# Kernel optimization log

Hardware: AMD Instinct MI355X
Metric: run time of the kernel (lower is better)

The kernel has to match this reference:

```python
import jax, jax.numpy as jnp
import numpy as np

EPS = 1e-9
LDIM = 4  # dim_g + dim_t + dim_b + dim_w


def _mvn_logpdf(v, F):
    # batched zero-mean multivariate normal log-density, v: (N,O), F: (N,O,O)
    chol = jnp.linalg.cholesky(F)
    z = jax.scipy.linalg.solve_triangular(chol, v[..., None], lower=True)[..., 0]
    quad = jnp.sum(z * z, axis=-1)
    logdet = 2.0 * jnp.sum(jnp.log(jnp.diagonal(chol, axis1=-2, axis2=-1)), axis=-1)
    k = v.shape[-1]
    return -0.5 * (quad + logdet + k * jnp.log(2.0 * jnp.pi))


def _forward(y, B_G, B_T, B_B, B_W, lambda_r1_free, lambda_r2_free,
             q_diag, r_diag, gamma1, gamma2_learnable):
    N, Nt, O = y.shape
    L = LDIM
    # ----- _build_matrices -----
    B11 = jnp.zeros((L, L)).at[0, 0].set(B_G[0, 0]).at[1, 1].set(B_T[0, 0]).at[2, 2].set(B_B[0, 0])
    B22 = jnp.zeros((L, L)).at[3, 3].set(B_W[0, 0])
    B12 = jnp.zeros((L, L)).at[3, :3].set(1.0 / 3.0)  # regime1 factors feed shared factor
    B21 = jnp.zeros((L, L))
    L1 = jnp.zeros((O, L))
    L1 = L1.at[0, 0].set(1.0).at[1, 0].set(lambda_r1_free[0]).at[2, 0].set(lambda_r1_free[1])
    L1 = L1.at[3, 1].set(1.0).at[4, 1].set(lambda_r1_free[2]).at[5, 1].set(lambda_r1_free[3])
    L1 = L1.at[6, 2].set(1.0).at[7, 2].set(lambda_r1_free[4]).at[8, 2].set(lambda_r1_free[5])
    L2 = jnp.zeros((O, L)).at[0, 3].set(1.0).at[1:, 3].set(lambda_r2_free)
    Q = jnp.diag(jnp.abs(q_diag) + 1e-4)
    R = jnp.diag(jnp.abs(r_diag) + 1e-4)
    F_JIT = 1e-5 * jnp.eye(O)
    I_L = jnp.eye(L)
    P22_CONST = 0.9999

    # ----- initial beliefs ('informative') -----
    prob0 = jnp.tile(jnp.array([0.99, 0.01], jnp.float32), (N, 1))
    eta0 = jnp.zeros((N, L), y.dtype)
    P0 = jnp.tile(jnp.diag(jnp.array([1000.0, 1000.0, 1000.0, 1e-9], y.dtype))[None], (N, 1, 1))

    def predict(B, eta, P):
        # eta: (N,L), P: (N,L,L)
        return eta @ B.T, jnp.einsum('ij,njk,lk->nil', B, P, B) + Q

    def innov(Lm, e, Pp, y_t):
        v = y_t - e @ Lm.T
        F = jnp.einsum('oi,nij,pj->nop', Lm, Pp, Lm) + R + F_JIT
        return v, F

    def kupdate(e, Pp, Lm, v, F):
        LP = jnp.einsum('oi,nij->noj', Lm, Pp)          # (N,O,L)
        K = jnp.swapaxes(jnp.linalg.solve(F, LP), -1, -2)  # P Lm^T F^{-1}, (N,L,O)
        e_u = e + jnp.einsum('nlo,no->nl', K, v)
        IKL = I_L - K @ Lm                                # (N,L,L)
        P_u = IKL @ Pp @ jnp.swapaxes(IKL, -1, -2) + jnp.einsum('nlo,op,nmp->nlm', K, R, K)
        return e_u, P_u

    def collapse(w_a, w_b, e_a, e_b, P_a, P_b):
        e = w_a[:, None] * e_a + w_b[:, None] * e_b
        da, db = e_a - e, e_b - e
        P = (w_a[:, None, None] * (P_a + da[:, :, None] * da[:, None, :])
             + w_b[:, None, None] * (P_b + db[:, :, None] * db[:, None, :]))
        return e, P

    def step(carry, y_t):
        prob, eta1, eta2, P1, P2, ll = carry
        # HMM transition: p11 depends on regime-1 state (first L-1 components)
        logit_p11 = gamma1 + eta1[:, :3] @ gamma2_learnable
        p11 = jax.nn.sigmoid(logit_p11)
        # predictions for the 4 regime transitions (origin -> destination)
        e11, Pp11 = predict(B11, eta1, P1)
        e12, Pp12 = predict(B21, eta2, P2)
        e21, Pp21 = predict(B12, eta1, P1)
        e22, Pp22 = predict(B22, eta2, P2)
        v11, F11 = innov(L1, e11, Pp11, y_t)
        v12, F12 = innov(L1, e12, Pp12, y_t)
        v21, F21 = innov(L2, e21, Pp21, y_t)
        v22, F22 = innov(L2, e22, Pp22, y_t)
        ll11 = _mvn_logpdf(v11, F11)
        ll12 = _mvn_logpdf(v12, F12)
        ll21 = _mvn_logpdf(v21, F21)
        ll22 = _mvn_logpdf(v22, F22)
        lp = jnp.log(prob + EPS)
        c11 = lp[:, 0] + jnp.log(p11 + EPS) + ll11
        c12 = lp[:, 1] + np.log(1.0 - P22_CONST + EPS) + ll12
        c21 = lp[:, 0] + jnp.log(1.0 - p11 + EPS) + ll21
        c22 = lp[:, 1] + np.log(P22_CONST + EPS) + ll22
        logp = jnp.stack([c11, c12, c21, c22], axis=1)
        ll_t = jax.scipy.special.logsumexp(logp, axis=1)
        pt = jnp.exp(logp - ll_t[:, None])
        pr1 = pt[:, 0] + pt[:, 1]
        pr2 = pt[:, 2] + pt[:, 3]
        W11 = pt[:, 0] / (pr1 + EPS)
        W12 = pt[:, 1] / (pr1 + EPS)
        W21 = pt[:, 2] / (pr2 + EPS)
        W22 = pt[:, 3] / (pr2 + EPS)
        eu11, Pu11 = kupdate(e11, Pp11, L1, v11, F11)
        eu12, Pu12 = kupdate(e12, Pp12, L1, v12, F12)
        eu21, Pu21 = kupdate(e21, Pp21, L2, v21, F21)
        eu22, Pu22 = kupdate(e22, Pp22, L2, v22, F22)
        eta1n, P1n = collapse(W11, W12, eu11, eu12, Pu11, Pu12)
        eta2n, P2n = collapse(W21, W22, eu21, eu22, Pu21, Pu22)
        probn = jnp.stack([pr1, pr2], axis=1)
        return (probn, eta1n, eta2n, P1n, P2n, ll + ll_t.sum()), None

    carry0 = (prob0, eta0, eta0, P0, P0, jnp.zeros((), y.dtype))
    (_, _, _, _, _, total_ll), _ = jax.lax.scan(step, carry0, jnp.swapaxes(y, 0, 1))
    return total_ll


def setup_inputs() -> dict:
    key = jax.random.key(0)
    ks = jax.random.split(key, 12)
    N, Nt, O = 16384, 64, 9
    f32 = jnp.float32
    return {
        'y': jax.random.normal(ks[0], (N, Nt, O), f32),
        'B_G': jax.random.uniform(ks[1], (1, 1), f32, 0.6, 0.95),  # Beta(5,1.5)-like AR coeffs
        'B_T': jax.random.uniform(ks[2], (1, 1), f32, 0.6, 0.95),
        'B_B': jax.random.uniform(ks[3], (1, 1), f32, 0.6, 0.95),
        'B_W': jax.random.uniform(ks[4], (1, 1), f32, 0.6, 0.95),
        'lambda_r1_free': jax.random.normal(ks[5], (6,), f32),
        'lambda_r2_free': jax.random.normal(ks[6], (O - 1,), f32),
        'q_diag': jax.random.uniform(ks[7], (LDIM,), f32),
        'r_diag': jax.random.uniform(ks[8], (O,), f32),
        'gamma1': jnp.abs(jax.random.normal(ks[9], (), f32)),
        'gamma2_learnable': jax.random.normal(ks[10], (LDIM - 1,), f32),
    }


def reference(y, B_G, B_T, B_B, B_W, lambda_r1_free, lambda_r2_free,
              q_diag, r_diag, gamma1, gamma2_learnable):
    return _forward(y, B_G, B_T, B_B, B_W, lambda_r1_free, lambda_r2_free,
                    q_diag, r_diag, gamma1, gamma2_learnable)
```

## Files before the change

### kernel.cpp

```cpp
#include <hip/hip_runtime.h>


typedef float v2f __attribute__((ext_vector_type(2)));

static __device__ __forceinline__ float frcp(float x)  { return __builtin_amdgcn_rcpf(x); }
static __device__ __forceinline__ float frsq(float x)  { return __builtin_amdgcn_rsqf(x); }
static __device__ __forceinline__ float fexp2(float x) { return __builtin_amdgcn_exp2f(x); }
static __device__ __forceinline__ float flog2(float x) { return __builtin_amdgcn_logf(x); }

template <int CTRL>
static __device__ __forceinline__ float dppf(float x) {
    int i = __float_as_int(x);
    i = __builtin_amdgcn_mov_dpp(i, CTRL, 0xF, 0xF, true);
    return __int_as_float(i);
}
#define ROTL 0xC9
#define ROTR 0xD2
#define XOR1 0xB1
#define XOR2 0x4E

static __device__ __forceinline__ float qsum(float x) {
    x += dppf<XOR1>(x);
    x += dppf<XOR2>(x);
    return x;
}

#define EPSF   1e-9f
#define L2E    1.4426950408889634f
#define LN2    0.6931471805599453f
#define L2_2PI_9 23.86346461225016f
#define C12F   1.00001e-4f
#define P22F   0.99990001f
#define QK     (-0.5f * L2E)

__global__ __launch_bounds__(64, 1)
void kf_kernel(const float* __restrict__ y,
               const float* __restrict__ pBG, const float* __restrict__ pBT,
               const float* __restrict__ pBB, const float* __restrict__ pBW,
               const float* __restrict__ lam1, const float* __restrict__ lam2,
               const float* __restrict__ qd,  const float* __restrict__ rd,
               const float* __restrict__ pG1, const float* __restrict__ pG2,
               float* __restrict__ partial, int N, int Nt)
{
    const int lane = threadIdx.x;
    const int j    = lane & 3;
    const int sid  = (blockIdx.x * 64 + lane) >> 2;
    const bool valid = (sid < N);
    const bool isRow = (j < 3);
    const int jj = isRow ? j : 0;
    const int rowlen = Nt * 9;
    const int nchunk = Nt / 4;

    const float bg = pBG[0], bt = pBT[0], bb = pBB[0], bw = pBW[0];
    float a[9], l2v[9], id[9], ld[9];
    a[0] = 1.f; a[1] = lam1[0]; a[2] = lam1[1];
    a[3] = 1.f; a[4] = lam1[2]; a[5] = lam1[3];
    a[6] = 1.f; a[7] = lam1[4]; a[8] = lam1[5];
    l2v[0] = 1.f;
    #pragma unroll
    for (int i = 0; i < 8; ++i) l2v[i + 1] = lam2[i];
    float l2detD = 0.f;
    #pragma unroll
    for (int o = 0; o < 9; ++o) {
        float dv = fabsf(rd[o]) + 1.0e-4f + 1.0e-5f;
        id[o] = 1.0f / dv;
        ld[o] = l2v[o] * id[o];
        l2detD += flog2(dv);
    }
    const float q0 = fabsf(qd[0]) + 1e-4f, q1 = fabsf(qd[1]) + 1e-4f;
    const float q2 = fabsf(qd[2]) + 1e-4f, q3 = fabsf(qd[3]) + 1e-4f;
    const float g0 = a[0]*a[0]*id[0] + a[1]*a[1]*id[1] + a[2]*a[2]*id[2];
    const float g1 = a[3]*a[3]*id[3] + a[4]*a[4]*id[4] + a[5]*a[5]*id[5];
    const float g2 = a[6]*a[6]*id[6] + a[7]*a[7]*id[7] + a[8]*a[8]*id[8];
    float h = 0.f;
    #pragma unroll
    for (int o = 0; o < 9; ++o) h += l2v[o] * ld[o];
    const float pk0 = q0 / (1.f + q0 * g0);
    const float pk1 = q1 / (1.f + q1 * g1);
    const float pk2 = q2 / (1.f + q2 * g2);
    const float C12D = C12F * frsq((1.f + q0*g0) * (1.f + q1*g1) * (1.f + q2*g2));
    const float gam1 = pG1[0], w0c = pG2[0], w1c = pG2[1], w2c = pG2[2];
    const float CC = -0.5f * (l2detD + L2_2PI_9);

    auto sel3 = [&](float x0, float x1, float x2) {
        float r = (jj == 1) ? x1 : x0;
        return (jj == 2) ? x2 : r;
    };
    const float aO0 = sel3(a[0], a[3], a[6]), aO1 = sel3(a[1], a[4], a[7]), aO2 = sel3(a[2], a[5], a[8]);
    const float iO0 = sel3(id[0], id[3], id[6]), iO1 = sel3(id[1], id[4], id[7]), iO2 = sel3(id[2], id[5], id[8]);
    const float lO0 = sel3(ld[0], ld[3], ld[6]), lO1 = sel3(ld[1], ld[4], ld[7]), lO2 = sel3(ld[2], ld[5], ld[8]);
    const float bS = sel3(bg, bt, bb), bN = sel3(bt, bb, bg), bP = sel3(bb, bg, bt);
    const float gS = sel3(g0, g1, g2), gN = sel3(g1, g2, g0), gP = sel3(g2, g0, g1);
    const float qS = sel3(q0, q1, q2);
    const float pkS = sel3(pk0, pk1, pk2);
    const float wS = sel3(w0c, w1c, w2c);

    auto z3 = [&](float x) { return isRow ? x : 0.0f; };

    float pf1 = 0.99f + EPSF, pf2 = 0.01f + EPSF;
    float seJ = 0.f;
    float Pr0 = 1000.f, Pr1 = 0.f, Pr2 = 0.f;
    float sm2 = 0.f, sp2 = 1e-9f;
    float acc2 = 0.0f;

    const float* row = y + (size_t)(valid ? sid : 0) * rowlen + 3 * jj;
    float A[12], B[12];
    auto loadChunk = [&](float (&buf)[12], int c) {
        const float* p = row + c * 36;
        #pragma unroll
        for (int s = 0; s < 4; ++s) {
            buf[s*3+0] = p[s*9+0];
            buf[s*3+1] = p[s*9+1];
            buf[s*3+2] = p[s*9+2];
        }
    };
    loadChunk(A, 0);

    auto step4 = [&](const float (&buf)[12]) {
        #pragma unroll
        for (int s = 0; s < 4; ++s) {
            const float y0 = buf[s*3+0], y1 = buf[s*3+1], y2 = buf[s*3+2];

            float logit = gam1 + qsum(z3(wS * seJ));
            float esig = fexp2(-logit * L2E);
            float p11 = frcp(1.f + esig);
            float pf11 = p11 + EPSF, pf21 = 1.f - p11 + EPSF;

            float epJ = bS * seJ;
            float S0 = bS*bS*Pr0 + qS;
            float S1 = bS*bN*Pr1;
            float S2 = bS*bP*Pr2;
            float M0 = S0*gS + 1.f;
            float M1 = S1*gN;
            float M2 = S2*gP;

            float v0 = y0 - aO0*epJ, v1 = y1 - aO1*epJ, v2 = y2 - aO2*epJ;
            float w0v = iO0*v0, w1v = iO1*v1, w2v = iO2*v2;
            float uJ = aO0*w0v + aO1*w1v + aO2*w2v;
            float vdv = qsum(z3(v0*w0v + v1*w1v + v2*w2v));
            float yl  = qsum(z3(lO0*y0 + lO1*y1 + lO2*y2));
            float ydy = vdv + qsum(z3(epJ * (2.f*uJ + gS*epJ)));

            float Mn0 = dppf<ROTL>(M0), Mn1 = dppf<ROTL>(M1), Mn2 = dppf<ROTL>(M2);
            float Mp0 = dppf<ROTR>(M0), Mp1 = dppf<ROTR>(M1), Mp2 = dppf<ROTR>(M2);
            float cf0 = Mn0*Mp0 - Mn1*Mp2;
            float cf1 = Mn1*Mp1 - Mn2*Mp0;
            float cf2 = Mn2*Mp2 - Mn0*Mp1;
            float det = M0*cf0 + M1*cf1 + M2*cf2;
            float rs  = frsq(det);
            float iM  = rs * rs;
            float cn0 = dppf<ROTL>(cf0), cn1 = dppf<ROTL>(cf1), cn2 = dppf<ROTL>(cf2);
            float cp0 = dppf<ROTR>(cf0), cp1 = dppf<ROTR>(cf1), cp2 = dppf<ROTR>(cf2);
            float Ci0 = iM * (S0*cf0 + S1*cn2 + S2*cp1);
            float Ci1 = iM * (S0*cf1 + S1*cn0 + S2*cp2);
            float Ci2 = iM * (S0*cf2 + S1*cn1 + S2*cp0);

            float uN = dppf<ROTL>(uJ), uP = dppf<ROTR>(uJ);
            float tJ = Ci0*uJ + Ci1*uN + Ci2*uP;
            float quad11 = vdv - qsum(z3(uJ * tJ));
            float euJ = epJ + tJ;

            float u12 = uJ + gS * epJ;
            float fJ  = pkS * u12;
            float quad12 = ydy - qsum(z3(pkS * u12 * u12));

            float seS = qsum(z3(seJ));
            float sP  = qsum(z3(Pr0 + Pr1 + Pr2));
            v2f m2v; m2v.x = seS * (1.f/3.f);       m2v.y = bw * sm2;
            v2f pvv; pvv.x = q3 + sP * (1.f/9.f);   pvv.y = bw*bw*sp2 + q3;
            v2f u1v  = (v2f){yl, yl} - m2v * (v2f){h, h};
            v2f vdav = (v2f){ydy, ydy} - m2v * ((v2f){2.f*yl, 2.f*yl} - m2v * (v2f){h, h});
            v2f denv = (v2f){1.f, 1.f} + pvv * (v2f){h, h};
            v2f rvv; rvv.x = frsq(denv.x); rvv.y = frsq(denv.y);
            v2f idev = rvv * rvv;
            v2f puv = pvv * idev;
            v2f quadv = vdav - puv * u1v * u1v;
            v2f euv = m2v + puv * u1v;

            float q11e = QK * quad11, q12e = QK * quad12;
            float q21e = QK * quadv.x, q22e = QK * quadv.y;
            float Mq = fmaxf(fmaxf(q11e, q12e), fmaxf(q21e, q22e));
            float w11 = pf1 * pf11 * rs    * fexp2(q11e - Mq);
            float w12 = pf2 * C12D         * fexp2(q12e - Mq);
            float w21 = pf1 * pf21 * rvv.x * fexp2(q21e - Mq);
            float w22 = pf2 * P22F * rvv.y * fexp2(q22e - Mq);
            float ssum = w11 + w12 + w21 + w22;
            acc2 += Mq + flog2(ssum);
            float pr1n = w11 + w12, pr2n = w21 + w22;
            float den1 = pr1n + EPSF * ssum, den2 = pr2n + EPSF * ssum;
            float inv1 = frcp(den1), inv2 = frcp(den2), issum = frcp(ssum);
            float W11 = w11*inv1, W12 = w12*inv1;
            float W21 = w21*inv2, W22 = w22*inv2;
            pf1 = pr1n * issum + EPSF;
            pf2 = pr2n * issum + EPSF;

            float neJ = W11*euJ + W12*fJ;
            float daJ = euJ - neJ, dbJ = fJ - neJ;
            float daN = dppf<ROTL>(daJ), daP = dppf<ROTR>(daJ);
            float dbN = dppf<ROTL>(dbJ), dbP = dppf<ROTR>(dbJ);
            Pr0 = W11*(Ci0 + daJ*daJ) + W12*(pkS + dbJ*dbJ);
            Pr1 = W11*(Ci1 + daJ*daN) + W12*(dbJ*dbN);
            Pr2 = W11*(Ci2 + daJ*daP) + W12*(dbJ*dbP);
            seJ = neJ;

            float nm2 = W21*euv.x + W22*euv.y;
            float dc = euv.x - nm2, dd = euv.y - nm2;
            sp2 = W21*(puv.x + dc*dc) + W22*(puv.y + dd*dd);
            sm2 = nm2;
        }
    };

    for (int c = 0; c < nchunk; c += 2) {
        if (c + 1 < nchunk) loadChunk(B, c + 1);
        step4(A);
        if (c + 2 < nchunk) loadChunk(A, c + 2);
        step4(B);
    }

    float acc = (valid && j == 0) ? (acc2 + (float)Nt * CC) * LN2 : 0.0f;
    #pragma unroll
    for (int off = 32; off; off >>= 1) acc += __shfl_down(acc, off, 64);
    if (lane == 0) partial[blockIdx.x] = acc;
}

__global__ __launch_bounds__(64)
void reduce_k(const float* __restrict__ part, float* __restrict__ out, int nb)
{
    float s = 0.f;
    for (int i = threadIdx.x; i < nb; i += 64) s += part[i];
    #pragma unroll
    for (int off = 32; off; off >>= 1) s += __shfl_down(s, off, 64);
    if (threadIdx.x == 0) out[0] = s;
}

extern "C" void kernel_launch(void* const* d_in, const int* in_sizes, int n_in,
                              void* d_out, int out_size, void* d_ws, size_t ws_size,
                              hipStream_t stream)
{
    const float* y    = (const float*)d_in[0];
    const float* pBG  = (const float*)d_in[1];
    const float* pBT  = (const float*)d_in[2];
    const float* pBB  = (const float*)d_in[3];
    const float* pBW  = (const float*)d_in[4];
    const float* lam1 = (const float*)d_in[5];
    const float* lam2 = (const float*)d_in[6];
    const float* qd   = (const float*)d_in[7];
    const float* rd   = (const float*)d_in[8];
    const float* pG1  = (const float*)d_in[9];
    const float* pG2  = (const float*)d_in[10];

    const int total = in_sizes[0];
    const int Nt = 64, O = 9;
    const int N = total / (Nt * O);
    const int blocks = (N * 4 + 63) / 64;

    float* partial = (float*)d_ws;
    kf_kernel<<<blocks, 64, 0, stream>>>(y, pBG, pBT, pBB, pBW, lam1, lam2,
                                         qd, rd, pG1, pG2, partial, N, Nt);
    reduce_k<<<1, 64, 0, stream>>>(partial, (float*)d_out, blocks);
}
```

Measured before the change: 126.7 us.

## Spread regime-pair weight computation across quad lanes and pair DPP reductions

The four regime-pair mixture weights are now computed one per lane in each 4-lane quad: a lane-selected exponent, determinant and transition factor, then a quad max and sum through DPP, and the normalized weights are broadcast back with quad_perm DPP. Independent quad reductions are paired into a two-wide helper so their DPP shuffles can be interleaved, and the rsqrt-then-square for inverses becomes a direct reciprocal. This is meant to cut the redundant per-lane transcendental work and the serialized reduction latency on the recurrence's critical path. In exchange it adds lane-dependent selects and more cross-lane dependencies, and it assumes the quad lane index j matches the intended regime layout.

```diff
diff --git a/kernel.cpp b/kernel.cpp
--- a/kernel.cpp
+++ b/kernel.cpp
@@ -18,10 +18,21 @@
 #define ROTR 0xD2
 #define XOR1 0xB1
 #define XOR2 0x4E
+#define BC0  0x00
+#define BC1  0x55
+#define BC2  0xAA
+#define BC3  0xFF
+#define P02  0x88
 
 static __device__ __forceinline__ float qsum(float x) {
     x += dppf<XOR1>(x);
     x += dppf<XOR2>(x);
+    return x;
+}
+static __device__ __forceinline__ v2f qsum2(v2f x) {
+    v2f t;
+    t.x = dppf<XOR1>(x.x); t.y = dppf<XOR1>(x.y); x += t;
+    t.x = dppf<XOR2>(x.x); t.y = dppf<XOR2>(x.y); x += t;
     return x;
 }
 
@@ -97,7 +108,7 @@
 
     auto z3 = [&](float x) { return isRow ? x : 0.0f; };
 
-    float pf1 = 0.99f + EPSF, pf2 = 0.01f + EPSF;
+    float pfl_use = ((j & 1) == 0 ? 0.99f : 0.01f) + EPSF;
     float seJ = 0.f;
     float Pr0 = 1000.f, Pr1 = 0.f, Pr2 = 0.f;
     float sm2 = 0.f, sp2 = 1e-9f;
@@ -121,10 +132,11 @@
         for (int s = 0; s < 4; ++s) {
             const float y0 = buf[s*3+0], y1 = buf[s*3+1], y2 = buf[s*3+2];
 
-            float logit = gam1 + qsum(z3(wS * seJ));
+            v2f r1 = qsum2((v2f){z3(wS * seJ), z3(seJ)});
+            float logit = gam1 + r1.x;
+            float seS = r1.y;
             float esig = fexp2(-logit * L2E);
             float p11 = frcp(1.f + esig);
-            float pf11 = p11 + EPSF, pf21 = 1.f - p11 + EPSF;
 
             float epJ = bS * seJ;
             float S0 = bS*bS*Pr0 + qS;
@@ -137,9 +149,13 @@
             float v0 = y0 - aO0*epJ, v1 = y1 - aO1*epJ, v2 = y2 - aO2*epJ;
             float w0v = iO0*v0, w1v = iO1*v1, w2v = iO2*v2;
             float uJ = aO0*w0v + aO1*w1v + aO2*w2v;
-            float vdv = qsum(z3(v0*w0v + v1*w1v + v2*w2v));
-            float yl  = qsum(z3(lO0*y0 + lO1*y1 + lO2*y2));
-            float ydy = vdv + qsum(z3(epJ * (2.f*uJ + gS*epJ)));
+            v2f r2 = qsum2((v2f){z3(v0*w0v + v1*w1v + v2*w2v),
+                                 z3(lO0*y0 + lO1*y1 + lO2*y2)});
+            float vdv = r2.x, yl = r2.y;
+            v2f r3 = qsum2((v2f){z3(epJ * (2.f*uJ + gS*epJ)),
+                                 z3(Pr0 + Pr1 + Pr2)});
+            float ydy = vdv + r3.x;
+            float sP = r3.y;
 
             float Mn0 = dppf<ROTL>(M0), Mn1 = dppf<ROTL>(M1), Mn2 = dppf<ROTL>(M2);
             float Mp0 = dppf<ROTR>(M0), Mp1 = dppf<ROTR>(M1), Mp2 = dppf<ROTR>(M2);
@@ -147,8 +163,7 @@
             float cf1 = Mn1*Mp1 - Mn2*Mp0;
             float cf2 = Mn2*Mp2 - Mn0*Mp1;
             float det = M0*cf0 + M1*cf1 + M2*cf2;
-            float rs  = frsq(det);
-            float iM  = rs * rs;
+            float iM  = frcp(det);
             float cn0 = dppf<ROTL>(cf0), cn1 = dppf<ROTL>(cf1), cn2 = dppf<ROTL>(cf2);
             float cp0 = dppf<ROTR>(cf0), cp1 = dppf<ROTR>(cf1), cp2 = dppf<ROTR>(cf2);
             float Ci0 = iM * (S0*cf0 + S1*cn2 + S2*cp1);
@@ -157,42 +172,46 @@
 
             float uN = dppf<ROTL>(uJ), uP = dppf<ROTR>(uJ);
             float tJ = Ci0*uJ + Ci1*uN + Ci2*uP;
-            float quad11 = vdv - qsum(z3(uJ * tJ));
-            float euJ = epJ + tJ;
-
             float u12 = uJ + gS * epJ;
             float fJ  = pkS * u12;
-            float quad12 = ydy - qsum(z3(pkS * u12 * u12));
-
-            float seS = qsum(z3(seJ));
-            float sP  = qsum(z3(Pr0 + Pr1 + Pr2));
+            v2f r4 = qsum2((v2f){z3(uJ * tJ), z3(pkS * u12 * u12)});
+            float quad11 = vdv - r4.x;
+            float quad12 = ydy - r4.y;
+            float euJ = epJ + tJ;
+
             v2f m2v; m2v.x = seS * (1.f/3.f);       m2v.y = bw * sm2;
             v2f pvv; pvv.x = q3 + sP * (1.f/9.f);   pvv.y = bw*bw*sp2 + q3;
             v2f u1v  = (v2f){yl, yl} - m2v * (v2f){h, h};
             v2f vdav = (v2f){ydy, ydy} - m2v * ((v2f){2.f*yl, 2.f*yl} - m2v * (v2f){h, h});
             v2f denv = (v2f){1.f, 1.f} + pvv * (v2f){h, h};
-            v2f rvv; rvv.x = frsq(denv.x); rvv.y = frsq(denv.y);
-            v2f idev = rvv * rvv;
+            v2f idev; idev.x = frcp(denv.x); idev.y = frcp(denv.y);
             v2f puv = pvv * idev;
             v2f quadv = vdav - puv * u1v * u1v;
             v2f euv = m2v + puv * u1v;
 
             float q11e = QK * quad11, q12e = QK * quad12;
             float q21e = QK * quadv.x, q22e = QK * quadv.y;
-            float Mq = fmaxf(fmaxf(q11e, q12e), fmaxf(q21e, q22e));
-            float w11 = pf1 * pf11 * rs    * fexp2(q11e - Mq);
-            float w12 = pf2 * C12D         * fexp2(q12e - Mq);
-            float w21 = pf1 * pf21 * rvv.x * fexp2(q21e - Mq);
-            float w22 = pf2 * P22F * rvv.y * fexp2(q22e - Mq);
-            float ssum = w11 + w12 + w21 + w22;
+            float q_l = (j == 0) ? q11e : (j == 1) ? q12e : (j == 2) ? q21e : q22e;
+            float Mq = q_l;
+            Mq = fmaxf(Mq, dppf<XOR1>(Mq));
+            Mq = fmaxf(Mq, dppf<XOR2>(Mq));
+            float det_l = (j == 0) ? det : (j == 2) ? denv.x : (j == 3) ? denv.y : 1.0f;
+            float hm = (j == 0) ? (p11 + EPSF)
+                     : (j == 1) ? C12D
+                     : (j == 2) ? (1.f - p11 + EPSF) : P22F;
+            float w_l = pfl_use * hm * frsq(det_l) * fexp2(q_l - Mq);
+            float ssum = qsum(w_l);
             acc2 += Mq + flog2(ssum);
-            float pr1n = w11 + w12, pr2n = w21 + w22;
-            float den1 = pr1n + EPSF * ssum, den2 = pr2n + EPSF * ssum;
-            float inv1 = frcp(den1), inv2 = frcp(den2), issum = frcp(ssum);
-            float W11 = w11*inv1, W12 = w12*inv1;
-            float W21 = w21*inv2, W22 = w22*inv2;
-            pf1 = pr1n * issum + EPSF;
-            pf2 = pr2n * issum + EPSF;
+            float wn = w_l + dppf<XOR1>(w_l);
+            float den_l = fmaf(EPSF, ssum, wn);
+            float W_l = w_l * frcp(den_l);
+            float issum = frcp(ssum);
+            float pfl = fmaf(wn, issum, EPSF);
+            pfl_use = dppf<P02>(pfl);
+            float W11 = dppf<BC0>(W_l);
+            float W12 = dppf<BC1>(W_l);
+            float W21 = dppf<BC2>(W_l);
+            float W22 = dppf<BC3>(W_l);
 
             float neJ = W11*euJ + W12*fJ;
             float daJ = euJ - neJ, dbJ = fJ - neJ;
```

After: 131.8 us. 4.1% more time.
